# Kernel optimization log

Hardware: AMD Instinct MI355X
Metric: run time of the kernel (lower is better)

Reference implementation:

```python
import jax, jax.numpy as jnp
import numpy as np

N_POINTS = 4


def bilinear_sample(feat, grid):
    """F.grid_sample(mode='bilinear', padding_mode='zeros', align_corners=True).
    feat: [B, C, H, W]; grid: [B, P, 2] with (x, y) in [-1, 1]. Returns [B, C, P].
    """
    B, C, H, W = feat.shape
    x = (grid[..., 0] + 1.0) * 0.5 * (W - 1)  # [B, P]
    y = (grid[..., 1] + 1.0) * 0.5 * (H - 1)
    x0 = jnp.floor(x); y0 = jnp.floor(y)
    x1 = x0 + 1.0;     y1 = y0 + 1.0
    wx1 = x - x0; wx0 = 1.0 - wx1
    wy1 = y - y0; wy0 = 1.0 - wy1
    featf = feat.reshape(B, C, H * W)

    def gather(xi, yi):
        valid = ((xi >= 0) & (xi <= W - 1) & (yi >= 0) & (yi <= H - 1)).astype(feat.dtype)
        xc = jnp.clip(xi, 0, W - 1).astype(jnp.int32)
        yc = jnp.clip(yi, 0, H - 1).astype(jnp.int32)
        idx = (yc * W + xc)[:, None, :]  # [B, 1, P]
        vals = jnp.take_along_axis(featf, jnp.broadcast_to(idx, (B, C, idx.shape[-1])), axis=2)
        return vals * valid[:, None, :]

    out = (gather(x0, y0) * (wx0 * wy0)[:, None, :]
           + gather(x1, y0) * (wx1 * wy0)[:, None, :]
           + gather(x0, y1) * (wx0 * wy1)[:, None, :]
           + gather(x1, y1) * (wx1 * wy1)[:, None, :])
    return out  # [B, C, P]


def setup_inputs() -> dict:
    key = jax.random.key(0)
    k1, k2, k3, k4 = jax.random.split(key, 4)
    BT, C, H, W, J = 64, 256, 64, 64, 17
    features = jax.random.normal(k1, (BT, C, H, W), dtype=jnp.float32)
    keypoint_coords = jax.random.uniform(k2, (BT, J, 2), dtype=jnp.float32, minval=-1.0, maxval=1.0)
    # offset predictor: 1x1 convs C->128->2N (final layer zero-init in torch; we use
    # small random weights so nonzero offsets exercise the deformable sampling path)
    w1 = jax.random.normal(k3, (128, C), dtype=jnp.float32) * (1.0 / np.sqrt(C))
    b1 = jnp.zeros((128,), dtype=jnp.float32)
    w2 = jax.random.normal(k4, (2 * N_POINTS, 128), dtype=jnp.float32) * 0.01
    b2 = jnp.zeros((2 * N_POINTS,), dtype=jnp.float32)
    return {"features": features, "keypoint_coords": keypoint_coords,
            "w1": w1, "b1": b1, "w2": w2, "b2": b2}


def reference(features, keypoint_coords, w1, b1, w2, b2):
    BT, C, H, W = features.shape
    J = keypoint_coords.shape[1]
    N = N_POINTS
    # seed features at the keypoints: [BT, C, J]
    seed = bilinear_sample(features, keypoint_coords)
    # 1x1-conv MLP predicting per-point offsets (pixels)
    h = jax.nn.relu(jnp.einsum('oc,bcj->boj', w1, seed) + b1[None, :, None])
    off = jnp.einsum('oh,bhj->boj', w2, h) + b2[None, :, None]  # [BT, 2N, J]
    off = off.transpose(0, 2, 1).reshape(BT, J, N, 2)
    # normalize pixel offsets to grid units
    scale = jnp.array([2.0 / (W - 1), 2.0 / (H - 1)], dtype=features.dtype)
    new_grid = keypoint_coords[:, :, None, :] + off * scale  # [BT, J, N, 2]
    samp = bilinear_sample(features, new_grid.reshape(BT, J * N, 2))  # [BT, C, J*N]
    out = samp.reshape(BT, C, J, N).transpose(0, 2, 3, 1).reshape(BT, J, N * C)
    return out
```

## Files before the change

### kernel.cpp

```cpp
#include <hip/hip_runtime.h>
#include <hip/hip_bf16.h>

#define BT 64
#define C  256
#define H  64
#define W  64
#define J  17
#define NP 4
#define HID 128

__device__ __forceinline__ float bilin_one(const float* __restrict__ p, float x, float y) {
    float x0f = floorf(x), y0f = floorf(y);
    int x0 = (int)x0f, y0 = (int)y0f;
    int x1 = x0 + 1,  y1 = y0 + 1;
    float wx1 = x - x0f, wx0 = 1.0f - wx1;
    float wy1 = y - y0f, wy0 = 1.0f - wy1;
    bool vx0 = ((unsigned)x0 < (unsigned)W);
    bool vx1 = ((unsigned)x1 < (unsigned)W);
    bool vy0 = ((unsigned)y0 < (unsigned)H);
    bool vy1 = ((unsigned)y1 < (unsigned)H);
    float v00 = (vx0 && vy0) ? p[y0 * W + x0] : 0.0f;
    float v10 = (vx1 && vy0) ? p[y0 * W + x1] : 0.0f;
    float v01 = (vx0 && vy1) ? p[y1 * W + x0] : 0.0f;
    float v11 = (vx1 && vy1) ? p[y1 * W + x1] : 0.0f;
    return v00 * (wx0 * wy0) + v10 * (wx1 * wy0)
         + v01 * (wx0 * wy1) + v11 * (wx1 * wy1);
}

__global__ __launch_bounds__(256) void adaptive_sampler_fused(
        const float* __restrict__ feat,
        const float* __restrict__ kp,
        const float* __restrict__ w1,
        const float* __restrict__ b1,
        const float* __restrict__ w2,
        const float* __restrict__ b2,
        float* __restrict__ out)
{
    const int bj  = blockIdx.x;
    const int b   = bj / J;
    const int tid = threadIdx.x;

    __shared__ float s_seed[C];
    __shared__ float s_h[HID];
    __shared__ float s_off[2 * NP];

    const float gx = kp[bj * 2 + 0];
    const float gy = kp[bj * 2 + 1];

    const float px = (gx + 1.0f) * 0.5f * (float)(W - 1);
    const float py = (gy + 1.0f) * 0.5f * (float)(H - 1);

    const float* fb = feat + (size_t)b * C * H * W;
    const float* plane = fb + (size_t)tid * H * W;

    s_seed[tid] = bilin_one(plane, px, py);
    __syncthreads();

    if (tid < HID) {
        const float4* wrow = (const float4*)(w1 + tid * C);
        float acc = 0.0f;
        #pragma unroll 8
        for (int c4 = 0; c4 < C / 4; ++c4) {
            float4 wv = wrow[c4];
            acc += wv.x * s_seed[c4 * 4 + 0];
            acc += wv.y * s_seed[c4 * 4 + 1];
            acc += wv.z * s_seed[c4 * 4 + 2];
            acc += wv.w * s_seed[c4 * 4 + 3];
        }
        s_h[tid] = fmaxf(acc + b1[tid], 0.0f);
    }
    __syncthreads();

    if (tid < 2 * NP) {
        const float4* wrow = (const float4*)(w2 + tid * HID);
        float acc = 0.0f;
        #pragma unroll 8
        for (int k4 = 0; k4 < HID / 4; ++k4) {
            float4 wv = wrow[k4];
            acc += wv.x * s_h[k4 * 4 + 0];
            acc += wv.y * s_h[k4 * 4 + 1];
            acc += wv.z * s_h[k4 * 4 + 2];
            acc += wv.w * s_h[k4 * 4 + 3];
        }
        s_off[tid] = acc + b2[tid];
    }
    __syncthreads();

    const float sx = 2.0f / (float)(W - 1);
    const float sy = 2.0f / (float)(H - 1);
    float* outp = out + (size_t)bj * NP * C + tid;
    #pragma unroll
    for (int n = 0; n < NP; ++n) {
        const float ngx = gx + s_off[2 * n + 0] * sx;
        const float ngy = gy + s_off[2 * n + 1] * sy;
        const float npx = (ngx + 1.0f) * 0.5f * (float)(W - 1);
        const float npy = (ngy + 1.0f) * 0.5f * (float)(H - 1);
        outp[n * C] = bilin_one(plane, npx, npy);
    }
}

extern "C" void kernel_launch(void* const* d_in, const int* in_sizes, int n_in,
                              void* d_out, int out_size, void* d_ws, size_t ws_size,
                              hipStream_t stream) {
    const float* feat = (const float*)d_in[0];
    const float* kp   = (const float*)d_in[1];
    const float* w1   = (const float*)d_in[2];
    const float* b1   = (const float*)d_in[3];
    const float* w2   = (const float*)d_in[4];
    const float* b2   = (const float*)d_in[5];
    float* out = (float*)d_out;

    dim3 grid(BT * J);
    dim3 block(256);
    adaptive_sampler_fused<<<grid, block, 0, stream>>>(feat, kp, w1, b1, w2, b2, out);
}
```

Before: 356.5 us.

## Split fused sampler into transpose, seed-MLP, and per-point sampling kernels

The single fused kernel becomes three launches. The first transposes w1 so each MLP thread reads it coalesced, the second computes the seed features, the MLP and the pixel coordinates into a workspace, and the third samples each offset point in its own block, giving four times as many blocks. The aim is to spread the scattered gathers over more blocks and remove the strided w1 row reads per thread. In exchange it adds two extra launches and a round trip of the coordinates through global memory.

```diff
diff --git a/kernel.cpp b/kernel.cpp
--- a/kernel.cpp
+++ b/kernel.cpp
@@ -27,14 +27,21 @@
          + v01 * (wx0 * wy1) + v11 * (wx1 * wy1);
 }
 
-__global__ __launch_bounds__(256) void adaptive_sampler_fused(
+__global__ __launch_bounds__(256) void ka_transpose_w1(
+        const float* __restrict__ w1, float* __restrict__ w1T) {
+    const int o = blockIdx.x;
+    const int c = threadIdx.x;
+    w1T[c * HID + o] = w1[o * C + c];
+}
+
+__global__ __launch_bounds__(256) void kb_seed_mlp(
         const float* __restrict__ feat,
         const float* __restrict__ kp,
-        const float* __restrict__ w1,
+        const float* __restrict__ w1T,
         const float* __restrict__ b1,
         const float* __restrict__ w2,
         const float* __restrict__ b2,
-        float* __restrict__ out)
+        float* __restrict__ coords)
 {
     const int bj  = blockIdx.x;
     const int b   = bj / J;
@@ -42,38 +49,29 @@
 
     __shared__ float s_seed[C];
     __shared__ float s_h[HID];
-    __shared__ float s_off[2 * NP];
 
     const float gx = kp[bj * 2 + 0];
     const float gy = kp[bj * 2 + 1];
-
     const float px = (gx + 1.0f) * 0.5f * (float)(W - 1);
     const float py = (gy + 1.0f) * 0.5f * (float)(H - 1);
 
-    const float* fb = feat + (size_t)b * C * H * W;
-    const float* plane = fb + (size_t)tid * H * W;
-
+    const float* plane = feat + ((size_t)b * C + tid) * (H * W);
     s_seed[tid] = bilin_one(plane, px, py);
     __syncthreads();
 
     if (tid < HID) {
-        const float4* wrow = (const float4*)(w1 + tid * C);
-        float acc = 0.0f;
+        float acc = b1[tid];
         #pragma unroll 8
-        for (int c4 = 0; c4 < C / 4; ++c4) {
-            float4 wv = wrow[c4];
-            acc += wv.x * s_seed[c4 * 4 + 0];
-            acc += wv.y * s_seed[c4 * 4 + 1];
-            acc += wv.z * s_seed[c4 * 4 + 2];
-            acc += wv.w * s_seed[c4 * 4 + 3];
+        for (int c = 0; c < C; ++c) {
+            acc += w1T[c * HID + tid] * s_seed[c];
         }
-        s_h[tid] = fmaxf(acc + b1[tid], 0.0f);
+        s_h[tid] = fmaxf(acc, 0.0f);
     }
     __syncthreads();
 
     if (tid < 2 * NP) {
         const float4* wrow = (const float4*)(w2 + tid * HID);
-        float acc = 0.0f;
+        float acc = b2[tid];
         #pragma unroll 8
         for (int k4 = 0; k4 < HID / 4; ++k4) {
             float4 wv = wrow[k4];
@@ -82,21 +80,31 @@
             acc += wv.z * s_h[k4 * 4 + 2];
             acc += wv.w * s_h[k4 * 4 + 3];
         }
-        s_off[tid] = acc + b2[tid];
+        const int axis = tid & 1;
+        const float g     = axis ? gy : gx;
+        const float scale = axis ? (2.0f / (float)(H - 1)) : (2.0f / (float)(W - 1));
+        const float dim1  = axis ? (float)(H - 1) : (float)(W - 1);
+        const float ng  = g + acc * scale;
+        const float pix = (ng + 1.0f) * 0.5f * dim1;
+        coords[bj * (2 * NP) + tid] = pix;
     }
-    __syncthreads();
+}
 
-    const float sx = 2.0f / (float)(W - 1);
-    const float sy = 2.0f / (float)(H - 1);
-    float* outp = out + (size_t)bj * NP * C + tid;
-    #pragma unroll
-    for (int n = 0; n < NP; ++n) {
-        const float ngx = gx + s_off[2 * n + 0] * sx;
-        const float ngy = gy + s_off[2 * n + 1] * sy;
-        const float npx = (ngx + 1.0f) * 0.5f * (float)(W - 1);
-        const float npy = (ngy + 1.0f) * 0.5f * (float)(H - 1);
-        outp[n * C] = bilin_one(plane, npx, npy);
-    }
+__global__ __launch_bounds__(256) void kc_sample(
+        const float* __restrict__ feat,
+        const float* __restrict__ coords,
+        float* __restrict__ out)
+{
+    const int id = blockIdx.x;
+    const int bj = id >> 2;
+    const int b  = bj / J;
+    const int c  = threadIdx.x;
+
+    const float px = coords[id * 2 + 0];
+    const float py = coords[id * 2 + 1];
+
+    const float* plane = feat + ((size_t)b * C + c) * (H * W);
+    out[(size_t)id * C + c] = bilin_one(plane, px, py);
 }
 
 extern "C" void kernel_launch(void* const* d_in, const int* in_sizes, int n_in,
@@ -110,7 +118,10 @@
     const float* b2   = (const float*)d_in[5];
     float* out = (float*)d_out;
 
-    dim3 grid(BT * J);
-    dim3 block(256);
-    adaptive_sampler_fused<<<grid, block, 0, stream>>>(feat, kp, w1, b1, w2, b2, out);
+    float* w1T    = (float*)d_ws;
+    float* coords = w1T + (size_t)C * HID;
+
+    ka_transpose_w1<<<dim3(HID), dim3(C), 0, stream>>>(w1, w1T);
+    kb_seed_mlp<<<dim3(BT * J), dim3(C), 0, stream>>>(feat, kp, w1T, b1, w2, b2, coords);
+    kc_sample<<<dim3(BT * J * NP), dim3(C), 0, stream>>>(feat, coords, out);
 }
```

Measured after the change: 366.6 us. +2.8%, slower.
